# Performance work log

Hardware: AMD Instinct MI355X
Metric: run time of the kernel (lower is better)

## Reference

```python
import jax, jax.numpy as jnp
import numpy as np

B, S, D_IN = 4, 2048, 1024
H, D_HEAD = 16, 64  # per-head output dim d_output=64


def setup_inputs() -> dict:
    key = jax.random.key(0)
    ks = jax.random.split(key, 9)
    s_in = 1.0 / np.sqrt(D_IN)
    s_o = 1.0 / np.sqrt(H * D_HEAD)
    return {
        "x": jax.random.normal(ks[0], (B, S, D_IN), dtype=jnp.float32),
        "Wq": jax.random.uniform(ks[1], (H, D_IN, D_HEAD), jnp.float32, -s_in, s_in),
        "bq": jax.random.uniform(ks[2], (H, D_HEAD), jnp.float32, -s_in, s_in),
        "Wk": jax.random.uniform(ks[3], (H, D_IN, D_HEAD), jnp.float32, -s_in, s_in),
        "bk": jax.random.uniform(ks[4], (H, D_HEAD), jnp.float32, -s_in, s_in),
        "Wv": jax.random.uniform(ks[5], (H, D_IN, D_HEAD), jnp.float32, -s_in, s_in),
        "bv": jax.random.uniform(ks[6], (H, D_HEAD), jnp.float32, -s_in, s_in),
        "Wo": jax.random.uniform(ks[7], (H * D_HEAD, D_HEAD), jnp.float32, -s_o, s_o),
        "bo": jax.random.uniform(ks[8], (D_HEAD,), jnp.float32, -s_o, s_o),
    }


def reference(x, Wq, bq, Wk, bk, Wv, bv, Wo, bo):
    # per-head projections: [B,H,S,Dh]
    q = jnp.einsum("bsd,hde->bhse", x, Wq) + bq[None, :, None, :]
    k = jnp.einsum("bsd,hde->bhse", x, Wk) + bk[None, :, None, :]
    v = jnp.einsum("bsd,hde->bhse", x, Wv) + bv[None, :, None, :]
    scale = 1.0 / np.sqrt(D_HEAD)
    scores = jnp.einsum("bhqe,bhke->bhqk", q, k) * scale  # [B,H,S,S]
    seq_len = x.shape[1]
    causal = jnp.tril(jnp.ones((seq_len, seq_len), dtype=bool))
    scores = jnp.where(causal[None, None], scores, -jnp.inf)
    attn = jax.nn.softmax(scores, axis=-1)  # dropout=0 -> identity
    out = jnp.einsum("bhqk,bhke->bhqe", attn, v)  # [B,H,S,Dh]
    # concat heads along feature dim (head order matches torch cat)
    out = out.transpose(0, 2, 1, 3).reshape(x.shape[0], seq_len, H * D_HEAD)
    return out @ Wo + bo
```

## Files before the change

### kernel.cpp

```cpp
#include <hip/hip_runtime.h>

typedef unsigned short u16;
typedef unsigned int u32;
typedef __attribute__((ext_vector_type(8))) short s16x8;
typedef __attribute__((ext_vector_type(4))) float f32x4;

#define MFMA(a,b,c) __builtin_amdgcn_mfma_f32_16x16x32_bf16((a),(b),(c),0,0,0)
#define QSCALE 0.18033688011112042f

#define BAR() do { asm volatile("" ::: "memory"); __builtin_amdgcn_s_barrier(); asm volatile("" ::: "memory"); } while(0)
#define WAITV(n) asm volatile("s_waitcnt vmcnt(" #n ")" ::: "memory")

__device__ __forceinline__ u16 bfc(float f){
  union { float f; unsigned int u; } c; c.f = f;
  return (u16)((c.u + 0x7fffu + ((c.u >> 16) & 1u)) >> 16);
}
__device__ __forceinline__ u32 pkbf(float lo, float hi){
  union { float f; u32 u; } a, b; a.f = lo; b.f = hi;
  return __builtin_amdgcn_perm(b.u + 0x8000u, a.u + 0x8000u, 0x07060302u);
}
__device__ __forceinline__ float fexp2(float x){ return __builtin_amdgcn_exp2f(x); }
__device__ __forceinline__ f32x4 zero4(){ f32x4 z; z[0]=0.f; z[1]=0.f; z[2]=0.f; z[3]=0.f; return z; }

__device__ __forceinline__ void gload_lds16(const u16* g, u16* l){
  __builtin_amdgcn_global_load_lds((const __attribute__((address_space(1))) unsigned int*)g,
                                   (__attribute__((address_space(3))) unsigned int*)l, 16, 0, 0);
}

__global__ __launch_bounds__(256) void k_cvt(const float* __restrict__ x, u16* __restrict__ xb){
  int i = (blockIdx.x * 256 + threadIdx.x) * 4;
  float4 v = *(const float4*)(x + i);
  *(uint2*)(xb + i) = make_uint2(pkbf(v.x, v.y), pkbf(v.z, v.w));
}

__global__ __launch_bounds__(256) void k_twp(const float* __restrict__ Wq, const float* __restrict__ Wk,
    const float* __restrict__ Wv, const float* __restrict__ Wo,
    u16* __restrict__ wt, u16* __restrict__ wot){
  __shared__ float t[64][65];
  int y = blockIdx.y, k0 = blockIdx.x * 64, tid = threadIdx.x;
  const float* src; u16* dst;
  if (y < 16)      { src = Wq + (size_t)y * 65536;        dst = wt + (size_t)y * 65536; }
  else if (y < 32) { src = Wk + (size_t)(y-16) * 65536;   dst = wt + (size_t)y * 65536; }
  else if (y < 48) { src = Wv + (size_t)(y-32) * 65536;   dst = wt + (size_t)y * 65536; }
  else             { src = Wo;                            dst = wot; }
  const float* s = src + (size_t)k0 * 64;
  int kl = tid >> 2, nc = (tid & 3) * 16;
  #pragma unroll
  for (int j = 0; j < 4; j++){
    float4 v = *(const float4*)(s + kl * 64 + nc + j * 4);
    t[kl][nc + j*4 + 0] = v.x; t[kl][nc + j*4 + 1] = v.y;
    t[kl][nc + j*4 + 2] = v.z; t[kl][nc + j*4 + 3] = v.w;
  }
  __syncthreads();
  int n = tid >> 2, kc = (tid & 3) * 16;
  u16 o[16];
  #pragma unroll
  for (int j = 0; j < 16; j++) o[j] = bfc(t[kc + j][n]);
  u16* d = dst + (size_t)n * 1024 + k0 + kc;
  *(uint4*)(d)     = *(uint4*)&o[0];
  *(uint4*)(d + 8) = *(uint4*)&o[8];
}

__global__ __launch_bounds__(256) void k_qkv(const u16* __restrict__ xb, const u16* __restrict__ wt,
    const float* __restrict__ bq, const float* __restrict__ bk, const float* __restrict__ bv,
    u16* __restrict__ Qo, u16* __restrict__ Ko, u16* __restrict__ VT){
  __shared__ u16 lds[24576];
  int tid = threadIdx.x, w = tid >> 6, lane = tid & 63;
  int l16 = lane & 15, g = lane >> 4;
  int row0 = blockIdx.x * 128, col0 = blockIdx.y * 128;
  int wm = (w & 1) * 64, wn = (w >> 1) * 64;
  f32x4 acc[4][4];
  #pragma unroll
  for (int mt = 0; mt < 4; mt++)
    #pragma unroll
    for (int nt = 0; nt < 4; nt++) acc[mt][nt] = zero4();

  int trow = tid >> 2;
  int lc = (tid & 3) ^ ((tid >> 3) & 3);
  const u16* gpa = xb + (size_t)(row0 + trow) * 1024 + lc * 8;
  const u16* gpb = wt + (size_t)(col0 + trow) * 1024 + lc * 8;

  int afo[4], bfo[4];
  #pragma unroll
  for (int mt = 0; mt < 4; mt++){
    int r = wm + mt * 16 + l16;
    afo[mt] = r * 32 + ((g ^ ((r >> 1) & 3)) * 8);
  }
  #pragma unroll
  for (int nt = 0; nt < 4; nt++){
    int r = wn + nt * 16 + l16;
    bfo[nt] = 4096 + r * 32 + ((g ^ ((r >> 1) & 3)) * 8);
  }

  auto stage = [&](int sl, int slot){
    u16* base = &lds[slot * 8192 + w * 512];
    int ko = sl * 32;
    gload_lds16(gpa + ko,             base);
    gload_lds16(gpa + ko + 64 * 1024, base + 2048);
    gload_lds16(gpb + ko,             base + 4096);
    gload_lds16(gpb + ko + 64 * 1024, base + 4096 + 2048);
  };
  auto compute = [&](int sel){
    s16x8 af[4], bf[4];
    #pragma unroll
    for (int mt = 0; mt < 4; mt++) af[mt] = *(const s16x8*)&lds[sel + afo[mt]];
    #pragma unroll
    for (int nt = 0; nt < 4; nt++) bf[nt] = *(const s16x8*)&lds[sel + bfo[nt]];
    __builtin_amdgcn_s_setprio(1);
    #pragma unroll
    for (int mt = 0; mt < 4; mt++)
      #pragma unroll
      for (int nt = 0; nt < 4; nt++) acc[mt][nt] = MFMA(af[mt], bf[nt], acc[mt][nt]);
    __builtin_amdgcn_s_setprio(0);
  };

  stage(0, 0); stage(1, 1);
  #pragma unroll 3
  for (int s = 0; s < 30; ++s){
    WAITV(4);
    BAR();
    stage(s + 2, (s + 2) % 3);
    compute((s % 3) * 8192);
  }
  WAITV(0); BAR();
  compute(0);
  compute(8192);

  #pragma unroll
  for (int nt = 0; nt < 4; nt++){
    int n = col0 + wn + nt * 16 + l16;
    int wi = n >> 10, hh = (n >> 6) & 15, dh = n & 63;
    const float* bptr = (wi == 0) ? bq : (wi == 1) ? bk : bv;
    float bval = bptr[hh * 64 + dh];
    #pragma unroll
    for (int mt = 0; mt < 4; mt++){
      int m0 = row0 + wm + mt * 16 + g * 4;
      int bb = m0 >> 11, ss = m0 & 2047;
      if (wi == 2){
        u32 p0 = pkbf(acc[mt][nt][0] + bval, acc[mt][nt][1] + bval);
        u32 p1 = pkbf(acc[mt][nt][2] + bval, acc[mt][nt][3] + bval);
        *(uint2*)&VT[(((size_t)bb * 16 + hh) * 64 + dh) * 2048 + ss] = make_uint2(p0, p1);
      } else {
        u16* dst = (wi == 0) ? Qo : Ko;
        float scl = (wi == 0) ? QSCALE : 1.0f;
        #pragma unroll
        for (int i = 0; i < 4; i++)
          dst[(((size_t)bb * 16 + hh) * 2048 + ss + i) * 64 + dh] = bfc((acc[mt][nt][i] + bval) * scl);
      }
    }
  }
}

__global__ __launch_bounds__(256, 3) void k_attn(const u16* __restrict__ Q, const u16* __restrict__ Kg,
    const u16* __restrict__ VT, u16* __restrict__ O){
  __shared__ u16 smem[18432];
  u16* Ks = smem;
  u16* Vt = smem + 4608;
  u16* Ps = smem + 9216;
  int hbi = blockIdx.x;
  int qt = 15 - (int)blockIdx.y;
  int b = hbi >> 4, h = hbi & 15;
  int tid = threadIdx.x, wave = tid >> 6, lane = tid & 63;
  int l16 = lane & 15, g = lane >> 4;
  size_t hb = (size_t)hbi * 2048 * 64;
  const u16* kbase = Kg + hb;
  const u16* vbase = VT + hb;
  int sr = tid >> 3, scc = (tid & 7) * 8;
  u16* PsW = Ps + wave * (32 * 72);
  int q0 = qt * 128 + wave * 32;
  s16x8 bq[2][2];
  #pragma unroll
  for (int j = 0; j < 2; j++)
    #pragma unroll
    for (int c = 0; c < 2; c++)
      bq[j][c] = *(const s16x8*)(Q + hb + (size_t)(q0 + j*16 + l16) * 64 + c*32 + g*8);
  f32x4 accO[4][2];
  #pragma unroll
  for (int mt = 0; mt < 4; mt++)
    #pragma unroll
    for (int j = 0; j < 2; j++) accO[mt][j] = zero4();
  float rs0 = 0.f, rs1 = 0.f;
  int nkt = 2 * qt + 2;
  uint4 ka0, ka1, va0, va1;
  ka0 = *(const uint4*)(kbase + (size_t)(sr)      * 64 + scc);
  ka1 = *(const uint4*)(kbase + (size_t)(sr + 32) * 64 + scc);
  va0 = *(const uint4*)(vbase + (size_t)(sr)      * 2048 + scc);
  va1 = *(const uint4*)(vbase + (size_t)(sr + 32) * 2048 + scc);
  *(uint4*)&Ks[sr * 72 + scc] = ka0; *(uint4*)&Ks[(sr + 32) * 72 + scc] = ka1;
  *(uint4*)&Vt[sr * 72 + scc] = va0; *(uint4*)&Vt[(sr + 32) * 72 + scc] = va1;
  __syncthreads();
  for (int kt = 0; kt < nkt; kt++){
    if (kt + 1 < nkt){
      int kb2 = (kt + 1) * 64;
      ka0 = *(const uint4*)(kbase + (size_t)(kb2 + sr)      * 64 + scc);
      ka1 = *(const uint4*)(kbase + (size_t)(kb2 + sr + 32) * 64 + scc);
      va0 = *(const uint4*)(vbase + (size_t)(sr)      * 2048 + kb2 + scc);
      va1 = *(const uint4*)(vbase + (size_t)(sr + 32) * 2048 + kb2 + scc);
    }
    int ks0 = kt * 64;
    if (ks0 <= q0 + 31){
      #pragma unroll
      for (int kb = 0; kb < 4; kb++){
        s16x8 ak0 = *(const s16x8*)&Ks[(kb*16 + l16) * 72 + g*8];
        s16x8 ak1 = *(const s16x8*)&Ks[(kb*16 + l16) * 72 + 32 + g*8];
        #pragma unroll
        for (int j = 0; j < 2; j++){
          f32x4 s = zero4();
          s = MFMA(ak0, bq[j][0], s);
          s = MFMA(ak1, bq[j][1], s);
          if (ks0 + kb*16 + 15 > q0 + j*16){
            int qrow = q0 + j*16 + l16;
            #pragma unroll
            for (int r = 0; r < 4; r++)
              if (ks0 + kb*16 + g*4 + r > qrow) s[r] = -1e30f;
          }
          float p0 = fexp2(s[0]), p1 = fexp2(s[1]), p2 = fexp2(s[2]), p3 = fexp2(s[3]);
          if (j == 0) rs0 += (p0 + p1) + (p2 + p3);
          else        rs1 += (p0 + p1) + (p2 + p3);
          *(uint2*)&PsW[(j*16 + l16) * 72 + kb*16 + g*4] = make_uint2(pkbf(p0, p1), pkbf(p2, p3));
        }
      }
      s16x8 av[4][2];
      #pragma unroll
      for (int mt = 0; mt < 4; mt++)
        #pragma unroll
        for (int kc = 0; kc < 2; kc++)
          av[mt][kc] = *(const s16x8*)&Vt[(mt*16 + l16) * 72 + kc*32 + g*8];
      #pragma unroll
      for (int j = 0; j < 2; j++){
        s16x8 bp0 = *(const s16x8*)&PsW[(j*16 + l16) * 72 + g*8];
        s16x8 bp1 = *(const s16x8*)&PsW[(j*16 + l16) * 72 + 32 + g*8];
        #pragma unroll
        for (int mt = 0; mt < 4; mt++){
          accO[mt][j] = MFMA(av[mt][0], bp0, accO[mt][j]);
          accO[mt][j] = MFMA(av[mt][1], bp1, accO[mt][j]);
        }
      }
    }
    if (kt + 1 < nkt){
      __syncthreads();
      *(uint4*)&Ks[sr * 72 + scc] = ka0; *(uint4*)&Ks[(sr + 32) * 72 + scc] = ka1;
      *(uint4*)&Vt[sr * 72 + scc] = va0; *(uint4*)&Vt[(sr + 32) * 72 + scc] = va1;
      __syncthreads();
    }
  }
  float rinv[2];
  #pragma unroll
  for (int j = 0; j < 2; j++){
    float l = (j == 0) ? rs0 : rs1;
    l += __shfl_xor(l, 16);
    l += __shfl_xor(l, 32);
    rinv[j] = 1.0f / l;
  }
  #pragma unroll
  for (int mt = 0; mt < 4; mt++)
    #pragma unroll
    for (int j = 0; j < 2; j++){
      float o0 = accO[mt][j][0] * rinv[j];
      float o1 = accO[mt][j][1] * rinv[j];
      float o2 = accO[mt][j][2] * rinv[j];
      float o3 = accO[mt][j][3] * rinv[j];
      *(uint2*)&O[((size_t)b * 2048 + q0 + j*16 + l16) * 1024 + h*64 + mt*16 + g*4] =
          make_uint2(pkbf(o0, o1), pkbf(o2, o3));
    }
}

__global__ __launch_bounds__(256) void k_oproj(const u16* __restrict__ Ob, const u16* __restrict__ wot,
    const float* __restrict__ bo, float* __restrict__ out){
  __shared__ u16 As[64][72];
  __shared__ u16 Bs[64][72];
  int rb = blockIdx.x, kc = blockIdx.y;
  int tid = threadIdx.x, wave = tid >> 6, lane = tid & 63;
  int l16 = lane & 15, g = lane >> 4;
  int wr = (wave & 1) * 32, wc = (wave >> 1) * 32;
  int row0 = rb * 64;
  f32x4 acc[2][2];
  acc[0][0]=zero4(); acc[0][1]=zero4(); acc[1][0]=zero4(); acc[1][1]=zero4();
  int r0s = tid >> 3, cc0 = (tid & 7) * 8, r1s = r0s + 32;
  for (int k0 = kc * 256; k0 < kc * 256 + 256; k0 += 64){
    __syncthreads();
    *(uint4*)&As[r0s][cc0] = *(const uint4*)(Ob + (size_t)(row0 + r0s) * 1024 + k0 + cc0);
    *(uint4*)&As[r1s][cc0] = *(const uint4*)(Ob + (size_t)(row0 + r1s) * 1024 + k0 + cc0);
    *(uint4*)&Bs[r0s][cc0] = *(const uint4*)(wot + (size_t)r0s * 1024 + k0 + cc0);
    *(uint4*)&Bs[r1s][cc0] = *(const uint4*)(wot + (size_t)r1s * 1024 + k0 + cc0);
    __syncthreads();
    #pragma unroll
    for (int c = 0; c < 2; c++){
      int kcc = c * 32;
      s16x8 a0 = *(const s16x8*)&As[wr      + l16][kcc + g * 8];
      s16x8 a1 = *(const s16x8*)&As[wr + 16 + l16][kcc + g * 8];
      s16x8 b0 = *(const s16x8*)&Bs[wc      + l16][kcc + g * 8];
      s16x8 b1 = *(const s16x8*)&Bs[wc + 16 + l16][kcc + g * 8];
      acc[0][0] = MFMA(a0, b0, acc[0][0]);
      acc[0][1] = MFMA(a0, b1, acc[0][1]);
      acc[1][0] = MFMA(a1, b0, acc[1][0]);
      acc[1][1] = MFMA(a1, b1, acc[1][1]);
    }
  }
  #pragma unroll
  for (int rt = 0; rt < 2; rt++){
    #pragma unroll
    for (int ct = 0; ct < 2; ct++){
      int col = wc + ct * 16 + l16;
      float bval = (kc == 0) ? bo[col] : 0.f;
      #pragma unroll
      for (int i = 0; i < 4; i++){
        int row = row0 + wr + rt * 16 + g * 4 + i;
        atomicAdd(&out[(size_t)row * 64 + col], acc[rt][ct][i] + bval);
      }
    }
  }
}

extern "C" void kernel_launch(void* const* d_in, const int* in_sizes, int n_in,
                              void* d_out, int out_size, void* d_ws, size_t ws_size,
                              hipStream_t stream){
  const float* x  = (const float*)d_in[0];
  const float* Wq = (const float*)d_in[1];
  const float* bq = (const float*)d_in[2];
  const float* Wk = (const float*)d_in[3];
  const float* bk = (const float*)d_in[4];
  const float* Wv = (const float*)d_in[5];
  const float* bv = (const float*)d_in[6];
  const float* Wo = (const float*)d_in[7];
  const float* bo = (const float*)d_in[8];

  u16* xb  = (u16*)d_ws;
  u16* wt  = xb  + 8388608;
  u16* wot = wt  + 3145728;
  u16* Qb  = wot + 65536;
  u16* Kb  = Qb  + 8388608;
  u16* VTb = Kb  + 8388608;
  u16* Ob  = xb;
  float* out = (float*)d_out;

  hipMemsetAsync(d_out, 0, (size_t)out_size * sizeof(float), stream);
  k_cvt<<<8192, 256, 0, stream>>>(x, xb);
  k_twp<<<dim3(16, 49), 256, 0, stream>>>(Wq, Wk, Wv, Wo, wt, wot);
  k_qkv<<<dim3(64, 24), 256, 0, stream>>>(xb, wt, bq, bk, bv, Qb, Kb, VTb);
  k_attn<<<dim3(64, 16), 256, 0, stream>>>(Qb, Kb, VTb, Ob);
  k_oproj<<<dim3(128, 4), 256, 0, stream>>>(Ob, wot, bo, out);
}
```

Measured before the change: 227.8 us.

## Fuse output projection into attention epilogue with per-head atomic accumulation

Removes the separate output-projection kernel. Each attention wave now stages its normalized bf16 output tile in its own LDS region, multiplies it by that head's slice of the transposed Wo with MFMA, and atomically adds the result into the fp32 output, with head 0 adding the bias. This avoids writing and re-reading the concatenated head output and saves one launch. In exchange, atomic traffic per output element rises to sixteen adds (one per head) and the attention epilogue does extra work.

```diff
diff --git a/kernel.cpp b/kernel.cpp
--- a/kernel.cpp
+++ b/kernel.cpp
@@ -152,7 +152,8 @@
 }
 
 __global__ __launch_bounds__(256, 3) void k_attn(const u16* __restrict__ Q, const u16* __restrict__ Kg,
-    const u16* __restrict__ VT, u16* __restrict__ O){
+    const u16* __restrict__ VT, const u16* __restrict__ wot,
+    const float* __restrict__ bo, float* __restrict__ out){
   __shared__ u16 smem[18432];
   u16* Ks = smem;
   u16* Vt = smem + 4608;
@@ -260,53 +261,32 @@
       float o1 = accO[mt][j][1] * rinv[j];
       float o2 = accO[mt][j][2] * rinv[j];
       float o3 = accO[mt][j][3] * rinv[j];
-      *(uint2*)&O[((size_t)b * 2048 + q0 + j*16 + l16) * 1024 + h*64 + mt*16 + g*4] =
-          make_uint2(pkbf(o0, o1), pkbf(o2, o3));
-    }
-}
-
-__global__ __launch_bounds__(256) void k_oproj(const u16* __restrict__ Ob, const u16* __restrict__ wot,
-    const float* __restrict__ bo, float* __restrict__ out){
-  __shared__ u16 As[64][72];
-  __shared__ u16 Bs[64][72];
-  int rb = blockIdx.x, kc = blockIdx.y;
-  int tid = threadIdx.x, wave = tid >> 6, lane = tid & 63;
-  int l16 = lane & 15, g = lane >> 4;
-  int wr = (wave & 1) * 32, wc = (wave >> 1) * 32;
-  int row0 = rb * 64;
-  f32x4 acc[2][2];
-  acc[0][0]=zero4(); acc[0][1]=zero4(); acc[1][0]=zero4(); acc[1][1]=zero4();
-  int r0s = tid >> 3, cc0 = (tid & 7) * 8, r1s = r0s + 32;
-  for (int k0 = kc * 256; k0 < kc * 256 + 256; k0 += 64){
-    __syncthreads();
-    *(uint4*)&As[r0s][cc0] = *(const uint4*)(Ob + (size_t)(row0 + r0s) * 1024 + k0 + cc0);
-    *(uint4*)&As[r1s][cc0] = *(const uint4*)(Ob + (size_t)(row0 + r1s) * 1024 + k0 + cc0);
-    *(uint4*)&Bs[r0s][cc0] = *(const uint4*)(wot + (size_t)r0s * 1024 + k0 + cc0);
-    *(uint4*)&Bs[r1s][cc0] = *(const uint4*)(wot + (size_t)r1s * 1024 + k0 + cc0);
-    __syncthreads();
-    #pragma unroll
-    for (int c = 0; c < 2; c++){
-      int kcc = c * 32;
-      s16x8 a0 = *(const s16x8*)&As[wr      + l16][kcc + g * 8];
-      s16x8 a1 = *(const s16x8*)&As[wr + 16 + l16][kcc + g * 8];
-      s16x8 b0 = *(const s16x8*)&Bs[wc      + l16][kcc + g * 8];
-      s16x8 b1 = *(const s16x8*)&Bs[wc + 16 + l16][kcc + g * 8];
-      acc[0][0] = MFMA(a0, b0, acc[0][0]);
-      acc[0][1] = MFMA(a0, b1, acc[0][1]);
-      acc[1][0] = MFMA(a1, b0, acc[1][0]);
-      acc[1][1] = MFMA(a1, b1, acc[1][1]);
-    }
-  }
-  #pragma unroll
-  for (int rt = 0; rt < 2; rt++){
-    #pragma unroll
-    for (int ct = 0; ct < 2; ct++){
-      int col = wc + ct * 16 + l16;
-      float bval = (kc == 0) ? bo[col] : 0.f;
-      #pragma unroll
-      for (int i = 0; i < 4; i++){
-        int row = row0 + wr + rt * 16 + g * 4 + i;
-        atomicAdd(&out[(size_t)row * 64 + col], acc[rt][ct][i] + bval);
+      *(uint2*)&PsW[(j*16 + l16) * 72 + mt*16 + g*4] = make_uint2(pkbf(o0, o1), pkbf(o2, o3));
+    }
+  s16x8 aw[4][2];
+  #pragma unroll
+  for (int nt = 0; nt < 4; nt++)
+    #pragma unroll
+    for (int kc = 0; kc < 2; kc++)
+      aw[nt][kc] = *(const s16x8*)(wot + (size_t)(nt*16 + l16) * 1024 + h*64 + kc*32 + g*8);
+  #pragma unroll
+  for (int j = 0; j < 2; j++){
+    s16x8 bp0 = *(const s16x8*)&PsW[(j*16 + l16) * 72 + g*8];
+    s16x8 bp1 = *(const s16x8*)&PsW[(j*16 + l16) * 72 + 32 + g*8];
+    int qrow = q0 + j*16 + l16;
+    #pragma unroll
+    for (int nt = 0; nt < 4; nt++){
+      f32x4 c = zero4();
+      c = MFMA(aw[nt][0], bp0, c);
+      c = MFMA(aw[nt][1], bp1, c);
+      float* op = out + ((size_t)b * 2048 + qrow) * 64 + nt*16 + g*4;
+      if (h == 0){
+        const float* bp = bo + nt*16 + g*4;
+        atomicAdd(op + 0, c[0] + bp[0]); atomicAdd(op + 1, c[1] + bp[1]);
+        atomicAdd(op + 2, c[2] + bp[2]); atomicAdd(op + 3, c[3] + bp[3]);
+      } else {
+        atomicAdd(op + 0, c[0]); atomicAdd(op + 1, c[1]);
+        atomicAdd(op + 2, c[2]); atomicAdd(op + 3, c[3]);
       }
     }
   }
@@ -331,13 +311,11 @@
   u16* Qb  = wot + 65536;
   u16* Kb  = Qb  + 8388608;
   u16* VTb = Kb  + 8388608;
-  u16* Ob  = xb;
   float* out = (float*)d_out;
 
   hipMemsetAsync(d_out, 0, (size_t)out_size * sizeof(float), stream);
   k_cvt<<<8192, 256, 0, stream>>>(x, xb);
   k_twp<<<dim3(16, 49), 256, 0, stream>>>(Wq, Wk, Wv, Wo, wt, wot);
   k_qkv<<<dim3(64, 24), 256, 0, stream>>>(xb, wt, bq, bk, bv, Qb, Kb, VTb);
-  k_attn<<<dim3(64, 16), 256, 0, stream>>>(Qb, Kb, VTb, Ob);
-  k_oproj<<<dim3(128, 4), 256, 0, stream>>>(Ob, wot, bo, out);
-}
+  k_attn<<<dim3(64, 16), 256, 0, stream>>>(Qb, Kb, VTb, wot, bo, out);
+}
```

Measured after the change: 291.4 us. 1.28x slower.
